# Performance work log

Measured on AMD Instinct MI355X. Metric: run time of the kernel, lower is better.

## Reference

```python
import jax, jax.numpy as jnp
import numpy as np

N_LEVELS = 16
F = 2
LOG2_T = 19
T = 1 << LOG2_T
BASE_RES = 16.0
FINEST_RES = 512.0
N_SAMPLES = 128
NEAR, FAR = 2.0, 6.0
BOX_MIN = jnp.array([-1.5, -1.5, -1.5], jnp.float32)
BOX_MAX = jnp.array([1.5, 1.5, 1.5], jnp.float32)
GEO_FEAT = 15
OUT_CH = 4

_PRIMES = np.array([1, 2654435761, 805459861], dtype=np.uint32)
_OFFSETS = np.array([[i, j, k] for i in (0, 1) for j in (0, 1) for k in (0, 1)], dtype=np.int32)  # [8,3]
_B = np.exp((np.log(FINEST_RES) - np.log(BASE_RES)) / (N_LEVELS - 1))
_RESOLUTIONS = np.floor(BASE_RES * _B ** np.arange(N_LEVELS)).astype(np.float32)


def setup_inputs() -> dict:
    key = jax.random.key(0)
    ks = jax.random.split(key, 10)
    n_rays = 16384
    o = jax.random.uniform(ks[0], (n_rays, 3), jnp.float32, -0.5, 0.5)
    d = jax.random.normal(ks[1], (n_rays, 3), jnp.float32)
    d = d / jnp.linalg.norm(d, axis=-1, keepdims=True)
    rays = jnp.concatenate([o, d], -1)
    hash_tables = jax.random.uniform(ks[2], (N_LEVELS, T, F), jnp.float32, -1e-4, 1e-4)
    def w(k, di, do):
        return jax.random.normal(k, (di, do), jnp.float32) * (1.0 / np.sqrt(di))
    return dict(
        rays=rays,
        hash_tables=hash_tables,
        ws0=w(ks[3], 32, 64), ws1=w(ks[4], 64, 64), ws2=w(ks[5], 64, 1 + GEO_FEAT),
        wc0=w(ks[6], 16 + GEO_FEAT, 64), wc1=w(ks[7], 64, 64), wc2=w(ks[8], 64, 64), wc3=w(ks[9], 64, OUT_CH - 1),
    )


def _hash_embed(x, tables):
    """Multi-res hash grid: x [P,3] world coords, tables [L,T,F] -> ([P,L*F], keep_mask [P])."""
    xc = jnp.clip(x, BOX_MIN, BOX_MAX)
    keep = jnp.all(x == xc, axis=-1)
    offs = jnp.asarray(_OFFSETS)          # [8,3]
    primes = jnp.asarray(_PRIMES)         # uint32
    feats = []
    for l in range(N_LEVELS):
        grid = (BOX_MAX - BOX_MIN) / _RESOLUTIONS[l]
        bl = jnp.floor((xc - BOX_MIN) / grid).astype(jnp.int32)   # [P,3] bottom-left voxel index
        vmin = bl.astype(jnp.float32) * grid + BOX_MIN
        wts = (xc - vmin) / grid                                  # trilinear weights [P,3]
        corners = (bl[:, None, :] + offs[None]).astype(jnp.uint32)  # [P,8,3]
        h = (corners[..., 0] * primes[0]) ^ (corners[..., 1] * primes[1]) ^ (corners[..., 2] * primes[2])
        idx = (h & jnp.uint32(T - 1)).astype(jnp.int32)           # [P,8]
        e = tables[l][idx]                                        # [P,8,F]
        w0, w1, w2 = wts[:, 0:1], wts[:, 1:2], wts[:, 2:3]
        c00 = e[:, 0] * (1 - w0) + e[:, 4] * w0
        c01 = e[:, 1] * (1 - w0) + e[:, 5] * w0
        c10 = e[:, 2] * (1 - w0) + e[:, 6] * w0
        c11 = e[:, 3] * (1 - w0) + e[:, 7] * w0
        c0 = c00 * (1 - w1) + c10 * w1
        c1 = c01 * (1 - w1) + c11 * w1
        feats.append(c0 * (1 - w2) + c1 * w2)
    return jnp.concatenate(feats, -1), keep


def _sh_encode(d):
    """Degree-4 spherical harmonics encoding, [P,3] -> [P,16]."""
    x, y, z = d[..., 0], d[..., 1], d[..., 2]
    xx, yy, zz = x * x, y * y, z * z
    xy, yz, xz = x * y, y * z, x * z
    C0 = 0.28209479177387814
    C1 = 0.4886025119029199
    C2 = (1.0925484305920792, -1.0925484305920792, 0.31539156525252005, -1.0925484305920792, 0.5462742152960396)
    C3 = (-0.5900435899266435, 2.890611442640554, -0.4570457994644658, 0.3731763325901154,
          -0.4570457994644658, 1.445305721320277, -0.5900435899266435)
    return jnp.stack([
        jnp.full_like(x, C0),
        -C1 * y, C1 * z, -C1 * x,
        C2[0] * xy, C2[1] * yz, C2[2] * (2.0 * zz - xx - yy), C2[3] * xz, C2[4] * (xx - yy),
        C3[0] * y * (3.0 * xx - yy), C3[1] * xy * z, C3[2] * y * (4.0 * zz - xx - yy),
        C3[3] * z * (2.0 * zz - 3.0 * xx - 3.0 * yy), C3[4] * x * (4.0 * zz - xx - yy),
        C3[5] * z * (xx - yy), C3[6] * x * (xx - 3.0 * yy),
    ], axis=-1)


def _forward(rays, hash_tables, ws0, ws1, ws2, wc0, wc1, wc2, wc3):
    n_rays = rays.shape[0]
    o, d = rays[:, :3], rays[:, 3:6]
    z = jnp.linspace(NEAR, FAR, N_SAMPLES, dtype=jnp.float32)
    zvals = jnp.broadcast_to(z, (n_rays, N_SAMPLES))
    pts = o[:, None, :] + d[:, None, :] * z[None, :, None]       # [N,S,3]
    P = n_rays * N_SAMPLES
    pts_f = pts.reshape(P, 3)
    dirs_f = jnp.broadcast_to(d[:, None, :], (n_rays, N_SAMPLES, 3)).reshape(P, 3)

    enc_pts, keep = _hash_embed(pts_f, hash_tables)              # [P,32], [P]
    enc_dirs = _sh_encode(dirs_f)                                # [P,16]

    # NeRFSmall: bias-free sigma net then color net
    h = jnp.maximum(enc_pts @ ws0, 0.0)
    h = jnp.maximum(h @ ws1, 0.0)
    h = h @ ws2                                                   # [P, 1+GEO_FEAT]
    sigma, geo = h[:, 0], h[:, 1:]
    hc = jnp.concatenate([enc_dirs, geo], -1)
    hc = jnp.maximum(hc @ wc0, 0.0)
    hc = jnp.maximum(hc @ wc1, 0.0)
    hc = jnp.maximum(hc @ wc2, 0.0)
    color = hc @ wc3                                              # [P, OUT_CH-1]

    sigma = jnp.where(keep, sigma, 0.0)                           # output[~keep_mask, -1] = 0
    raw = jnp.concatenate([color, sigma[:, None]], -1).reshape(n_rays, N_SAMPLES, OUT_CH)

    # Integrator (raw2outputs)
    dists = zvals[:, 1:] - zvals[:, :-1]
    dists = jnp.concatenate([dists, jnp.full((n_rays, 1), 1e10, jnp.float32)], -1)
    dists = dists * jnp.linalg.norm(d, axis=-1, keepdims=True)
    chs = jax.nn.sigmoid(raw[..., :-1])
    alpha = 1.0 - jnp.exp(-jnp.maximum(raw[..., -1], 0.0) * dists)
    trans = jnp.cumprod(1.0 - alpha + 1e-10, axis=-1)
    trans = jnp.concatenate([jnp.ones((n_rays, 1), jnp.float32), trans[:, :-1]], -1)
    weights = alpha * trans
    chs_map = jnp.einsum('ns,nsc->nc', weights, chs)
    depth_map = jnp.sum(weights * zvals, -1)
    probs = jnp.concatenate([weights, 1.0 - jnp.sum(weights, -1, keepdims=True) + 1e-6], -1)
    p = probs / jnp.sum(probs, -1, keepdims=True)
    sparsity_loss = -jnp.sum(p * jnp.log(jnp.clip(p, 1e-37)), -1)
    return chs_map, depth_map, sparsity_loss


def reference(rays, hash_tables, ws0, ws1, ws2, wc0, wc1, wc2, wc3):
    return _forward(rays, hash_tables, ws0, ws1, ws2, wc0, wc1, wc2, wc3)
```

## Files before the change

kernel.cpp:

```cpp
#include <hip/hip_runtime.h>

#define NRAYS 16384
#define NLEV  16
#define THASH 524288
#define MAXACT 48
#define MAXPTS (NRAYS*MAXACT)
#define MBLK  256
#define MGRID 1024

__device__ __forceinline__ float zval32(int i) {
  const float step = 4.0f / 127.0f;
  return __fadd_rn(2.0f, __fmul_rn((float)i, step));
}
__device__ __forceinline__ float pcoord(float o, float d, float z) {
  return __fadd_rn(o, __fmul_rn(d, z));
}

__global__ __launch_bounds__(64)
void k_classify(const float* __restrict__ rays,
                float* __restrict__ sh,
                unsigned* __restrict__ counter,
                unsigned* __restrict__ rbase,
                unsigned* __restrict__ rn,
                unsigned* __restrict__ plist) {
  int lane = threadIdx.x;
  int r = blockIdx.x * 64 + lane;
  if (r >= NRAYS) return;
  float ox = rays[6*r+0], oy = rays[6*r+1], oz = rays[6*r+2];
  float dx = rays[6*r+3], dy = rays[6*r+4], dz = rays[6*r+5];
  float x = dx, y = dy, z = dz;
  float xx = x*x, yy = y*y, zz = z*z, xy = x*y, yz = y*z, xz = x*z;
  float* shp = sh + 16*r;
  shp[0]  = 0.28209479177387814f;
  shp[1]  = -0.4886025119029199f * y;
  shp[2]  =  0.4886025119029199f * z;
  shp[3]  = -0.4886025119029199f * x;
  shp[4]  =  1.0925484305920792f * xy;
  shp[5]  = -1.0925484305920792f * yz;
  shp[6]  =  0.31539156525252005f * (2.0f*zz - xx - yy);
  shp[7]  = -1.0925484305920792f * xz;
  shp[8]  =  0.5462742152960396f * (xx - yy);
  shp[9]  = -0.5900435899266435f * y * (3.0f*xx - yy);
  shp[10] =  2.890611442640554f  * xy * z;
  shp[11] = -0.4570457994644658f * y * (4.0f*zz - xx - yy);
  shp[12] =  0.3731763325901154f * z * (2.0f*zz - 3.0f*xx - 3.0f*yy);
  shp[13] = -0.4570457994644658f * x * (4.0f*zz - xx - yy);
  shp[14] =  1.445305721320277f  * z * (xx - yy);
  shp[15] = -0.5900435899266435f * x * (xx - 3.0f*yy);
  unsigned n = 0;
  for (int i = 0; i < 128; ++i) {
    float zi = zval32(i);
    float px = pcoord(ox, dx, zi);
    float py = pcoord(oy, dy, zi);
    float pz = pcoord(oz, dz, zi);
    bool in = (px >= -1.5f) && (px <= 1.5f) && (py >= -1.5f) && (py <= 1.5f)
           && (pz >= -1.5f) && (pz <= 1.5f);
    if (!in) break;
    ++n;
  }
  unsigned pre = n;
#pragma unroll
  for (int d = 1; d < 64; d <<= 1) {
    unsigned v = __shfl_up(pre, d, 64);
    if (lane >= d) pre += v;
  }
  unsigned excl  = pre - n;
  unsigned total = __shfl(pre, 63, 64);
  unsigned base0 = 0;
  if (lane == 0) base0 = atomicAdd(counter, total);
  base0 = __shfl(base0, 0, 64);
  unsigned base = base0 + excl;
  rbase[r] = base;
  rn[r]    = n;
  for (unsigned i = 0; i < n; ++i) plist[base + i] = (unsigned)(r*128 + (int)i);
}

template<int IN, int TOTOUT, int JC, bool RELU>
__device__ __forceinline__ void layer(const float* __restrict__ W, int jbase,
                                      const float* __restrict__ in,
                                      float* __restrict__ out, int lane) {
  float acc[JC];
#pragma unroll
  for (int j = 0; j < JC; ++j) acc[j] = 0.0f;
#pragma unroll 4
  for (int k = 0; k < IN; ++k) {
    float a = in[k*64 + lane];
    const float* Wk = W + k*TOTOUT + jbase;
#pragma unroll
    for (int j = 0; j < JC; ++j) acc[j] = fmaf(a, Wk[j], acc[j]);
  }
#pragma unroll
  for (int j = 0; j < JC; ++j)
    out[(jbase + j)*64 + lane] = RELU ? fmaxf(acc[j], 0.0f) : acc[j];
}

__global__ __launch_bounds__(MBLK)
void k_mlp(const float* __restrict__ rays,
           const float* __restrict__ tables,
           const float* __restrict__ w_s0, const float* __restrict__ w_s1,
           const float* __restrict__ w_s2, const float* __restrict__ w_c0,
           const float* __restrict__ w_c1, const float* __restrict__ w_c2,
           const float* __restrict__ w_c3,
           const float* __restrict__ sh,
           const unsigned* __restrict__ counter,
           const unsigned* __restrict__ plist,
           float4* __restrict__ results) {
  __shared__ float A[64*64];
  __shared__ float B[64*64];
  __shared__ float sig_s[64];
  const int t = threadIdx.x;
  const int lane = t & 63;
  const int q = __builtin_amdgcn_readfirstlane(t >> 6);
  const unsigned count = *counter;
  const unsigned ntiles = (count + 63u) >> 6;
  const float RESF[NLEV] = {16.f,20.f,25.f,32.f,40.f,50.f,64.f,80.f,
                            101.f,128.f,161.f,203.f,256.f,322.f,406.f,512.f};
  for (unsigned tile = blockIdx.x; tile < ntiles; tile += MGRID) {
    unsigned s = (tile << 6) + (unsigned)lane;
    unsigned pid = (s < count) ? plist[s] : 0u;
    int r = (int)(pid >> 7);
    int i = (int)(pid & 127u);
    {
      float zi = zval32(i);
      float px = pcoord(rays[6*r+0], rays[6*r+3], zi);
      float py = pcoord(rays[6*r+1], rays[6*r+4], zi);
      float pz = pcoord(rays[6*r+2], rays[6*r+5], zi);
      float xcx = fminf(fmaxf(px, -1.5f), 1.5f);
      float xcy = fminf(fmaxf(py, -1.5f), 1.5f);
      float xcz = fminf(fmaxf(pz, -1.5f), 1.5f);
#pragma unroll
      for (int li = 0; li < 4; ++li) {
        int l = 4*q + li;
        const float grid = 3.0f / RESF[l];
        float bfx = floorf(__fdiv_rn(__fadd_rn(xcx, 1.5f), grid));
        float bfy = floorf(__fdiv_rn(__fadd_rn(xcy, 1.5f), grid));
        float bfz = floorf(__fdiv_rn(__fadd_rn(xcz, 1.5f), grid));
        float vmx = __fadd_rn(__fmul_rn(bfx, grid), -1.5f);
        float vmy = __fadd_rn(__fmul_rn(bfy, grid), -1.5f);
        float vmz = __fadd_rn(__fmul_rn(bfz, grid), -1.5f);
        float wx = __fdiv_rn(__fsub_rn(xcx, vmx), grid);
        float wy = __fdiv_rn(__fsub_rn(xcy, vmy), grid);
        float wz = __fdiv_rn(__fsub_rn(xcz, vmz), grid);
        unsigned cx0 = (unsigned)(int)bfx, cy0 = (unsigned)(int)bfy, cz0 = (unsigned)(int)bfz;
        unsigned cx1 = cx0 + 1u, cy1 = cy0 + 1u, cz1 = cz0 + 1u;
        unsigned hy0 = cy0*2654435761u, hy1 = cy1*2654435761u;
        unsigned hz0 = cz0*805459861u,  hz1 = cz1*805459861u;
        const float2* tb = (const float2*)tables + (size_t)l*THASH;
        float2 e000 = tb[(cx0^hy0^hz0)&(THASH-1)];
        float2 e001 = tb[(cx0^hy0^hz1)&(THASH-1)];
        float2 e010 = tb[(cx0^hy1^hz0)&(THASH-1)];
        float2 e011 = tb[(cx0^hy1^hz1)&(THASH-1)];
        float2 e100 = tb[(cx1^hy0^hz0)&(THASH-1)];
        float2 e101 = tb[(cx1^hy0^hz1)&(THASH-1)];
        float2 e110 = tb[(cx1^hy1^hz0)&(THASH-1)];
        float2 e111 = tb[(cx1^hy1^hz1)&(THASH-1)];
        float iwx = 1.f-wx, iwy = 1.f-wy, iwz = 1.f-wz;
        float c00a = e000.x*iwx + e100.x*wx, c00b = e000.y*iwx + e100.y*wx;
        float c01a = e001.x*iwx + e101.x*wx, c01b = e001.y*iwx + e101.y*wx;
        float c10a = e010.x*iwx + e110.x*wx, c10b = e010.y*iwx + e110.y*wx;
        float c11a = e011.x*iwx + e111.x*wx, c11b = e011.y*iwx + e111.y*wx;
        float c0a = c00a*iwy + c10a*wy, c0b = c00b*iwy + c10b*wy;
        float c1a = c01a*iwy + c11a*wy, c1b = c01b*iwy + c11b*wy;
        A[(2*l+0)*64 + lane] = c0a*iwz + c1a*wz;
        A[(2*l+1)*64 + lane] = c0b*iwz + c1b*wz;
      }
    }
    __syncthreads();
    layer<32,64,16,true >(w_s0, q*16, A, B, lane); __syncthreads();
    layer<64,64,16,true >(w_s1, q*16, B, A, lane); __syncthreads();
    layer<64,16, 4,false>(w_s2, q*4,  A, B, lane); __syncthreads();
    if (q == 0) sig_s[lane] = B[0*64 + lane];
    for (int idx = t; idx < 31*64; idx += MBLK) {
      int k = idx >> 6, p = idx & 63;
      float v;
      if (k < 16) {
        unsigned sp = (tile << 6) + (unsigned)p;
        unsigned pp = (sp < count) ? plist[sp] : 0u;
        v = sh[(pp >> 7)*16 + k];
      } else {
        v = B[(k-15)*64 + p];
      }
      A[idx] = v;
    }
    __syncthreads();
    layer<31,64,16,true >(w_c0, q*16, A, B, lane); __syncthreads();
    layer<64,64,16,true >(w_c1, B ? q*16 : 0, B, A, lane); __syncthreads();
    layer<64,64,16,true >(w_c2, q*16, A, B, lane); __syncthreads();
    if (q < 3) layer<64,3,1,false>(w_c3, q, B, A, lane);
    __syncthreads();
    if (q == 0 && s < count) {
      float4 res;
      res.x = sig_s[lane];
      res.y = A[0*64 + lane];
      res.z = A[1*64 + lane];
      res.w = A[2*64 + lane];
      results[s] = res;
    }
    __syncthreads();
  }
}

__global__ __launch_bounds__(64)
void k_comp(const float* __restrict__ rays,
            const unsigned* __restrict__ rbase,
            const unsigned* __restrict__ rn,
            const float4* __restrict__ results,
            float* __restrict__ out) {
  int r = blockIdx.x * 64 + threadIdx.x;
  if (r >= NRAYS) return;
  float dx = rays[6*r+3], dy = rays[6*r+4], dz = rays[6*r+5];
  float dnorm = sqrtf(dx*dx + dy*dy + dz*dz);
  int n = (int)rn[r];
  unsigned base = rbase[r];
  const float step = 4.0f/127.0f;
  const float diststep = __fmul_rn(step, dnorm);
  float S = 0.f, ch0 = 0.f, ch1 = 0.f, ch2 = 0.f, dep = 0.f, trans = 1.f;
  for (int i = 0; i < n; ++i) {
    float4 rs = results[base + i];
    float z = zval32(i);
    float sg = fmaxf(rs.x, 0.f);
    float alpha = -expm1f(-__fmul_rn(sg, diststep));
    float w = __fmul_rn(alpha, trans);
    trans = __fmul_rn(trans, __fadd_rn(__fsub_rn(1.f, alpha), 1e-10f));
    float s0 = 1.f/(1.f + expf(-rs.y));
    float s1 = 1.f/(1.f + expf(-rs.z));
    float s2 = 1.f/(1.f + expf(-rs.w));
    S += w; ch0 += w*s0; ch1 += w*s1; ch2 += w*s2; dep += w*z;
  }
  float rem  = __fadd_rn(__fsub_rn(1.f, S), 1e-6f);
  float Stot = __fadd_rn(S, rem);
  float loss = 0.f, trans2 = 1.f;
  for (int i = 0; i < n; ++i) {
    float4 rs = results[base + i];
    float sg = fmaxf(rs.x, 0.f);
    float alpha = -expm1f(-__fmul_rn(sg, diststep));
    float w = __fmul_rn(alpha, trans2);
    trans2 = __fmul_rn(trans2, __fadd_rn(__fsub_rn(1.f, alpha), 1e-10f));
    float p = __fdiv_rn(w, Stot);
    loss += p * logf(fmaxf(p, 1e-37f));
  }
  float pl = __fdiv_rn(rem, Stot);
  loss += pl * logf(fmaxf(pl, 1e-37f));
  out[3*r+0] = ch0; out[3*r+1] = ch1; out[3*r+2] = ch2;
  out[3*NRAYS + r] = dep;
  out[4*NRAYS + r] = -loss;
}

extern "C" void kernel_launch(void* const* d_in, const int* in_sizes, int n_in,
                              void* d_out, int out_size, void* d_ws, size_t ws_size,
                              hipStream_t stream) {
  const float* rays   = (const float*)d_in[0];
  const float* tables = (const float*)d_in[1];
  const float* ws0    = (const float*)d_in[2];
  const float* ws1    = (const float*)d_in[3];
  const float* ws2    = (const float*)d_in[4];
  const float* wc0    = (const float*)d_in[5];
  const float* wc1    = (const float*)d_in[6];
  const float* wc2    = (const float*)d_in[7];
  const float* wc3    = (const float*)d_in[8];

  char* ws = (char*)d_ws;
  unsigned* counter = (unsigned*)ws;
  unsigned* rbase   = (unsigned*)(ws + 256);
  unsigned* rn      = (unsigned*)(ws + 256 + 65536);
  float*    sh      = (float*)  (ws + 256 + 131072);
  float4*   results = (float4*) (ws + 1179904);
  unsigned* plist   = (unsigned*)(ws + 1179904 + (size_t)MAXPTS*16);

  hipMemsetAsync(counter, 0, 4, stream);
  k_classify<<<NRAYS/64, 64, 0, stream>>>(rays, sh, counter, rbase, rn, plist);
  k_mlp<<<MGRID, MBLK, 0, stream>>>(rays, tables, ws0, ws1, ws2,
                                    wc0, wc1, wc2, wc3, sh, counter, plist, results);
  k_comp<<<NRAYS/64, 64, 0, stream>>>(rays, rbase, rn, results, (float*)d_out);
}
```

Measured before the change: 187.9 us.

## Transpose MLP layer mapping: lanes over output neurons, warps over point groups

Changes the MLP layer so each lane computes one output neuron for 16 points, reading weights with a coalesced per-lane load and activations as broadcast float4 LDS reads from a padded (stride 68) transposed layout. Before, each lane owned a point and read 16 uniform weights per k. Also adds a min-blocks occupancy hint to launch_bounds. The narrow layers (16 and 3 outputs) leave most lanes idle, and the wider shared arrays raise LDS use.

Result: slower. 218.0 us (+16.0%).

```diff
diff --git a/kernel.cpp b/kernel.cpp
--- a/kernel.cpp
+++ b/kernel.cpp
@@ -7,6 +7,7 @@
 #define MAXPTS (NRAYS*MAXACT)
 #define MBLK  256
 #define MGRID 1024
+#define STR   68
 
 __device__ __forceinline__ float zval32(int i) {
   const float step = 4.0f / 127.0f;
@@ -75,26 +76,43 @@
   for (unsigned i = 0; i < n; ++i) plist[base + i] = (unsigned)(r*128 + (int)i);
 }
 
-template<int IN, int TOTOUT, int JC, bool RELU>
-__device__ __forceinline__ void layer(const float* __restrict__ W, int jbase,
-                                      const float* __restrict__ in,
-                                      float* __restrict__ out, int lane) {
-  float acc[JC];
-#pragma unroll
-  for (int j = 0; j < JC; ++j) acc[j] = 0.0f;
-#pragma unroll 4
-  for (int k = 0; k < IN; ++k) {
-    float a = in[k*64 + lane];
-    const float* Wk = W + k*TOTOUT + jbase;
-#pragma unroll
-    for (int j = 0; j < JC; ++j) acc[j] = fmaf(a, Wk[j], acc[j]);
-  }
-#pragma unroll
-  for (int j = 0; j < JC; ++j)
-    out[(jbase + j)*64 + lane] = RELU ? fmaxf(acc[j], 0.0f) : acc[j];
-}
-
-__global__ __launch_bounds__(MBLK)
+template<int IN, int TOTOUT, bool RELU>
+__device__ __forceinline__ void layerT(const float* __restrict__ W,
+                                       const float* __restrict__ Ain,
+                                       float* __restrict__ Bout,
+                                       int lane, int pb) {
+  if (lane < TOTOUT) {
+    float acc[16];
+#pragma unroll
+    for (int p = 0; p < 16; ++p) acc[p] = 0.0f;
+#pragma unroll 2
+    for (int k = 0; k < IN; ++k) {
+      float w = W[k*TOTOUT + lane];
+      const float4* ar = (const float4*)(Ain + k*STR + pb);
+      float4 a0 = ar[0], a1 = ar[1], a2 = ar[2], a3 = ar[3];
+      acc[ 0] = fmaf(w, a0.x, acc[ 0]); acc[ 1] = fmaf(w, a0.y, acc[ 1]);
+      acc[ 2] = fmaf(w, a0.z, acc[ 2]); acc[ 3] = fmaf(w, a0.w, acc[ 3]);
+      acc[ 4] = fmaf(w, a1.x, acc[ 4]); acc[ 5] = fmaf(w, a1.y, acc[ 5]);
+      acc[ 6] = fmaf(w, a1.z, acc[ 6]); acc[ 7] = fmaf(w, a1.w, acc[ 7]);
+      acc[ 8] = fmaf(w, a2.x, acc[ 8]); acc[ 9] = fmaf(w, a2.y, acc[ 9]);
+      acc[10] = fmaf(w, a2.z, acc[10]); acc[11] = fmaf(w, a2.w, acc[11]);
+      acc[12] = fmaf(w, a3.x, acc[12]); acc[13] = fmaf(w, a3.y, acc[13]);
+      acc[14] = fmaf(w, a3.z, acc[14]); acc[15] = fmaf(w, a3.w, acc[15]);
+    }
+    float4* br = (float4*)(Bout + lane*STR + pb);
+#pragma unroll
+    for (int c = 0; c < 4; ++c) {
+      float4 v;
+      v.x = RELU ? fmaxf(acc[4*c+0], 0.0f) : acc[4*c+0];
+      v.y = RELU ? fmaxf(acc[4*c+1], 0.0f) : acc[4*c+1];
+      v.z = RELU ? fmaxf(acc[4*c+2], 0.0f) : acc[4*c+2];
+      v.w = RELU ? fmaxf(acc[4*c+3], 0.0f) : acc[4*c+3];
+      br[c] = v;
+    }
+  }
+}
+
+__global__ __launch_bounds__(MBLK, 4)
 void k_mlp(const float* __restrict__ rays,
            const float* __restrict__ tables,
            const float* __restrict__ w_s0, const float* __restrict__ w_s1,
@@ -105,12 +123,13 @@
            const unsigned* __restrict__ counter,
            const unsigned* __restrict__ plist,
            float4* __restrict__ results) {
-  __shared__ float A[64*64];
-  __shared__ float B[64*64];
+  __shared__ __align__(16) float A[64*STR];
+  __shared__ __align__(16) float B[64*STR];
   __shared__ float sig_s[64];
   const int t = threadIdx.x;
   const int lane = t & 63;
   const int q = __builtin_amdgcn_readfirstlane(t >> 6);
+  const int pb = q*16;
   const unsigned count = *counter;
   const unsigned ntiles = (count + 63u) >> 6;
   const float RESF[NLEV] = {16.f,20.f,25.f,32.f,40.f,50.f,64.f,80.f,
@@ -161,15 +180,15 @@
         float c11a = e011.x*iwx + e111.x*wx, c11b = e011.y*iwx + e111.y*wx;
         float c0a = c00a*iwy + c10a*wy, c0b = c00b*iwy + c10b*wy;
         float c1a = c01a*iwy + c11a*wy, c1b = c01b*iwy + c11b*wy;
-        A[(2*l+0)*64 + lane] = c0a*iwz + c1a*wz;
-        A[(2*l+1)*64 + lane] = c0b*iwz + c1b*wz;
+        A[(2*l+0)*STR + lane] = c0a*iwz + c1a*wz;
+        A[(2*l+1)*STR + lane] = c0b*iwz + c1b*wz;
       }
     }
     __syncthreads();
-    layer<32,64,16,true >(w_s0, q*16, A, B, lane); __syncthreads();
-    layer<64,64,16,true >(w_s1, q*16, B, A, lane); __syncthreads();
-    layer<64,16, 4,false>(w_s2, q*4,  A, B, lane); __syncthreads();
-    if (q == 0) sig_s[lane] = B[0*64 + lane];
+    layerT<32,64,true >(w_s0, A, B, lane, pb); __syncthreads();
+    layerT<64,64,true >(w_s1, B, A, lane, pb); __syncthreads();
+    layerT<64,16,false>(w_s2, A, B, lane, pb); __syncthreads();
+    if (t < 64) sig_s[t] = B[0*STR + t];
     for (int idx = t; idx < 31*64; idx += MBLK) {
       int k = idx >> 6, p = idx & 63;
       float v;
@@ -178,23 +197,27 @@
         unsigned pp = (sp < count) ? plist[sp] : 0u;
         v = sh[(pp >> 7)*16 + k];
       } else {
-        v = B[(k-15)*64 + p];
+        v = B[(k-15)*STR + p];
       }
-      A[idx] = v;
-    }
-    __syncthreads();
-    layer<31,64,16,true >(w_c0, q*16, A, B, lane); __syncthreads();
-    layer<64,64,16,true >(w_c1, B ? q*16 : 0, B, A, lane); __syncthreads();
-    layer<64,64,16,true >(w_c2, q*16, A, B, lane); __syncthreads();
-    if (q < 3) layer<64,3,1,false>(w_c3, q, B, A, lane);
-    __syncthreads();
-    if (q == 0 && s < count) {
-      float4 res;
-      res.x = sig_s[lane];
-      res.y = A[0*64 + lane];
-      res.z = A[1*64 + lane];
-      res.w = A[2*64 + lane];
-      results[s] = res;
+      A[k*STR + p] = v;
+    }
+    __syncthreads();
+    layerT<31,64,true >(w_c0, A, B, lane, pb); __syncthreads();
+    layerT<64,64,true >(w_c1, B, A, lane, pb); __syncthreads();
+    layerT<64,64,true >(w_c2, A, B, lane, pb); __syncthreads();
+    layerT<64, 3,false>(w_c3, B, A, lane, pb);
+    __syncthreads();
+    if (lane < 16) {
+      int p = pb + lane;
+      unsigned ss = (tile << 6) + (unsigned)p;
+      if (ss < count) {
+        float4 res;
+        res.x = sig_s[p];
+        res.y = A[0*STR + p];
+        res.z = A[1*STR + p];
+        res.w = A[2*STR + p];
+        results[ss] = res;
+      }
     }
     __syncthreads();
   }
```
